# Kernel tuning notes

Hardware: AMD Instinct MI355X
Metric: run time of the kernel (lower is better)

## Reference

```python
import jax, jax.numpy as jnp
import numpy as np

N, IN_F, OUT_F = 2048, 512, 512

def setup_inputs() -> dict:
    key = jax.random.key(0)
    kx, ka, kb = jax.random.split(key, 3)
    x = jax.random.uniform(kx, (N, IN_F), dtype=jnp.float32)          # inputs in [0,1]
    a = jax.random.uniform(ka, (OUT_F, IN_F), dtype=jnp.float32)      # weight in [0,1]
    b = jax.random.uniform(kb, (OUT_F,), dtype=jnp.float32)           # bias in [0,1]
    return {"x": x, "a": a, "b": b}

def reference(x, a, b):
    # Lukasiewicz / max-plus 'matmul':
    # y[n,o] = max(0, max_i(x[n,i] + a[o,i] - 1)), then max with bias b[o].
    inter = x[:, None, :] + a[None, :, :] - 1.0        # [N, out, in]
    y = jnp.maximum(jnp.max(inter, axis=-1), 0.0)      # [N, out]
    y = jnp.maximum(y, b[None, :])
    return y
```

## Files before the change

### kernel.cpp

```cpp
#include <hip/hip_runtime.h>
#include <cstdint>


#define NROW 2048
#define NK   512
#define NCOL 512
#define RPB  8
#define CBL  256
#define KQ   32
typedef float f32x4 __attribute__((ext_vector_type(4)));

__device__ __forceinline__ void async_load16(const float* g, float* l) {
  __builtin_amdgcn_global_load_lds(
      (const __attribute__((address_space(1))) void*)g,
      (__attribute__((address_space(3))) void*)l, 16, 0, 0);
}

__global__ __launch_bounds__(256) void luka_prep(const float* __restrict__ A,
                                                 f32x4* __restrict__ Apc) {
  int idx = blockIdx.x * 256 + threadIdx.x;
  int o  = idx >> 7;
  int k4 = idx & 127;
  int cb = o >> 8, oc = o & 255;
  int c  = oc >> 6, l = oc & 63;
  f32x4 v = *(const f32x4*)(A + o * NK + k4 * 4);
  Apc[((cb * 128 + k4) << 8) + (l << 2) + c] = v;
}

__global__ __launch_bounds__(256) void luka_main(
    const f32x4* __restrict__ Apc, const float* __restrict__ X,
    const float* __restrict__ Bv, float* __restrict__ Y) {
  __shared__ float xsl[RPB * NK];
  __shared__ float red[4 * RPB * CBL];
  const int tid  = threadIdx.x;
  const int lane = tid & 63;
  const int w    = tid >> 6;
  const int colblk  = blockIdx.x;
  const int rowBase = blockIdx.y * RPB;

  {
    const float* Xg = X + (size_t)rowBase * NK;
#pragma unroll
    for (int rnd = 0; rnd < 4; ++rnd) {
      int base = rnd * 256 + w * 64;
      async_load16(Xg + (size_t)(base + lane) * 4, &xsl[base * 4]);
    }
  }

  const f32x4* __restrict__ Aw =
      Apc + (((size_t)(colblk * 128 + w * KQ)) << 8) + (lane << 2);

  float acc[RPB][4];
#pragma unroll
  for (int r = 0; r < RPB; ++r)
#pragma unroll
    for (int c = 0; c < 4; ++c) acc[r][c] = 0.0f;

  f32x4 a0 = __builtin_nontemporal_load(Aw + 0);
  f32x4 a1 = __builtin_nontemporal_load(Aw + 1);
  f32x4 a2 = __builtin_nontemporal_load(Aw + 2);
  f32x4 a3 = __builtin_nontemporal_load(Aw + 3);

  __syncthreads();

#pragma unroll 2
  for (int j = 0; j < KQ; ++j) {
    f32x4 n0, n1, n2, n3;
    if (j + 1 < KQ) {
      const f32x4* p = Aw + ((j + 1) << 8);
      n0 = __builtin_nontemporal_load(p + 0);
      n1 = __builtin_nontemporal_load(p + 1);
      n2 = __builtin_nontemporal_load(p + 2);
      n3 = __builtin_nontemporal_load(p + 3);
    }
    const int kb = (w * KQ + j) * 4;
#pragma unroll
    for (int r = 0; r < RPB; ++r) {
      const f32x4 xv = *(const f32x4*)&xsl[r * NK + kb];
      f32x4 s0 = a0 + xv;
      f32x4 s1 = a1 + xv;
      f32x4 s2 = a2 + xv;
      f32x4 s3 = a3 + xv;
      acc[r][0] = fmaxf(fmaxf(s0.x, s0.y), acc[r][0]);
      acc[r][0] = fmaxf(fmaxf(s0.z, s0.w), acc[r][0]);
      acc[r][1] = fmaxf(fmaxf(s1.x, s1.y), acc[r][1]);
      acc[r][1] = fmaxf(fmaxf(s1.z, s1.w), acc[r][1]);
      acc[r][2] = fmaxf(fmaxf(s2.x, s2.y), acc[r][2]);
      acc[r][2] = fmaxf(fmaxf(s2.z, s2.w), acc[r][2]);
      acc[r][3] = fmaxf(fmaxf(s3.x, s3.y), acc[r][3]);
      acc[r][3] = fmaxf(fmaxf(s3.z, s3.w), acc[r][3]);
    }
    a0 = n0; a1 = n1; a2 = n2; a3 = n3;
  }

#pragma unroll
  for (int r = 0; r < RPB; ++r)
#pragma unroll
    for (int c = 0; c < 4; ++c)
      red[(w * RPB + r) * CBL + c * 64 + lane] = acc[r][c];
  __syncthreads();

  const float bv = Bv[colblk * CBL + tid];
#pragma unroll
  for (int p = 0; p < RPB; ++p) {
    float m = fmaxf(fmaxf(red[(0 * RPB + p) * CBL + tid],
                          red[(1 * RPB + p) * CBL + tid]),
                    fmaxf(red[(2 * RPB + p) * CBL + tid],
                          red[(3 * RPB + p) * CBL + tid]));
    float t = m - 1.0f;
    Y[(size_t)(rowBase + p) * NCOL + colblk * CBL + tid] =
        fmaxf(fmaxf(t, bv), 0.0f);
  }
}

#define TILE 64
#define BK   64
__global__ __launch_bounds__(256) void luka_fb(
    const float* __restrict__ X, const float* __restrict__ A,
    const float* __restrict__ Bv, float* __restrict__ Y) {
  __shared__ float xs[2][TILE * BK];
  __shared__ float as[2][TILE * BK];
  const int tid = threadIdx.x, wave = tid >> 6, tx = tid & 15, ty = tid >> 4;
  const int rowBase = blockIdx.y * TILE, colBase = blockIdx.x * TILE;
  uint32_t xoff[4], aoff[4];
#pragma unroll
  for (int r = 0; r < 4; ++r) {
    int row = ty * 4 + r;
    xoff[r] = (uint32_t)row * 256u + ((uint32_t)((row & 15) ^ (row >> 2)) << 4);
  }
#pragma unroll
  for (int c = 0; c < 4; ++c) {
    int row = tx * 4 + c;
    aoff[c] = (uint32_t)row * 256u + ((uint32_t)((row & 15) ^ (row >> 2)) << 4);
  }
  float acc[4][4];
#pragma unroll
  for (int r = 0; r < 4; ++r)
#pragma unroll
    for (int c = 0; c < 4; ++c) acc[r][c] = 0.0f;
  const int row0 = tid >> 4, sl = tid & 15;
  auto stage = [&](int buf, int kt) {
#pragma unroll
    for (int j = 0; j < 4; ++j) {
      int row = row0 + j * 16;
      int m = (row & 15) ^ (row >> 2);
      int kk = ((sl ^ m) << 2);
      async_load16(X + (size_t)(rowBase + row) * NK + kt * BK + kk,
                   &xs[buf][j * 1024 + wave * 256]);
      async_load16(A + (size_t)(colBase + row) * NK + kt * BK + kk,
                   &as[buf][j * 1024 + wave * 256]);
    }
  };
  stage(0, 0);
  __syncthreads();
  int buf = 0;
#pragma unroll 1
  for (int kt = 0; kt < NK / BK; ++kt) {
    if (kt < NK / BK - 1) stage(buf ^ 1, kt + 1);
    const char* xb = (const char*)&xs[buf][0];
    const char* ab = (const char*)&as[buf][0];
#pragma unroll
    for (int s4 = 0; s4 < BK / 4; ++s4) {
      f32x4 xf[4], af[4];
#pragma unroll
      for (int r = 0; r < 4; ++r)
        xf[r] = *(const f32x4*)(xb + (xoff[r] ^ (uint32_t)(s4 << 4)));
#pragma unroll
      for (int c = 0; c < 4; ++c)
        af[c] = *(const f32x4*)(ab + (aoff[c] ^ (uint32_t)(s4 << 4)));
#pragma unroll
      for (int r = 0; r < 4; ++r)
#pragma unroll
        for (int c = 0; c < 4; ++c) {
          f32x4 s = xf[r] + af[c];
          float t0 = fmaxf(fmaxf(s.x, s.y), acc[r][c]);
          acc[r][c] = fmaxf(fmaxf(s.z, s.w), t0);
        }
    }
    __syncthreads();
    buf ^= 1;
  }
  const f32x4 bv = *(const f32x4*)&Bv[colBase + tx * 4];
  float bvv[4] = {bv.x, bv.y, bv.z, bv.w};
#pragma unroll
  for (int r = 0; r < 4; ++r) {
    f32x4 o;
    o.x = fmaxf(fmaxf(acc[r][0] - 1.0f, bvv[0]), 0.0f);
    o.y = fmaxf(fmaxf(acc[r][1] - 1.0f, bvv[1]), 0.0f);
    o.z = fmaxf(fmaxf(acc[r][2] - 1.0f, bvv[2]), 0.0f);
    o.w = fmaxf(fmaxf(acc[r][3] - 1.0f, bvv[3]), 0.0f);
    *(f32x4*)&Y[(size_t)(rowBase + ty * 4 + r) * NCOL + colBase + tx * 4] = o;
  }
}

extern "C" void kernel_launch(void* const* d_in, const int* in_sizes, int n_in,
                              void* d_out, int out_size, void* d_ws, size_t ws_size,
                              hipStream_t stream) {
  const float* X = (const float*)d_in[0];
  const float* A = (const float*)d_in[1];
  const float* B = (const float*)d_in[2];
  float* Y = (float*)d_out;

  if (ws_size >= (size_t)NCOL * NK * sizeof(float)) {
    f32x4* Apc = (f32x4*)d_ws;
    luka_prep<<<dim3(NCOL * NK / 4 / 256), dim3(256), 0, stream>>>(A, Apc);
    dim3 grid(NCOL / CBL, NROW / RPB);
    luka_main<<<grid, dim3(256), 0, stream>>>(Apc, X, B, Y);
  } else {
    dim3 grid(NCOL / TILE, NROW / TILE);
    luka_fb<<<grid, dim3(256), 0, stream>>>(X, A, B, Y);
  }
}
```

Before: 99.41 us.

## Assign one row per wave over full K, drop LDS cross-wave reduction

Instead of splitting the K dimension across the four waves and reducing their partial maxima through shared memory, each wave now handles one output row over the full K range, with 4 rows per block. This removes the reduction buffer, the second barrier and the strided output pass, and doubles the grid size. In exchange each wave streams the whole A column block with ordinary rather than nontemporal loads, so A traffic per block rises and there is less register-level reuse of each A load across rows.

```diff
diff --git a/kernel.cpp b/kernel.cpp
--- a/kernel.cpp
+++ b/kernel.cpp
@@ -5,9 +5,8 @@
 #define NROW 2048
 #define NK   512
 #define NCOL 512
-#define RPB  8
+#define RPB  4
 #define CBL  256
-#define KQ   32
 typedef float f32x4 __attribute__((ext_vector_type(4)));
 
 __device__ __forceinline__ void async_load16(const float* g, float* l) {
@@ -31,7 +30,6 @@
     const f32x4* __restrict__ Apc, const float* __restrict__ X,
     const float* __restrict__ Bv, float* __restrict__ Y) {
   __shared__ float xsl[RPB * NK];
-  __shared__ float red[4 * RPB * CBL];
   const int tid  = threadIdx.x;
   const int lane = tid & 63;
   const int w    = tid >> 6;
@@ -41,76 +39,54 @@
   {
     const float* Xg = X + (size_t)rowBase * NK;
 #pragma unroll
-    for (int rnd = 0; rnd < 4; ++rnd) {
+    for (int rnd = 0; rnd < 2; ++rnd) {
       int base = rnd * 256 + w * 64;
       async_load16(Xg + (size_t)(base + lane) * 4, &xsl[base * 4]);
     }
   }
 
   const f32x4* __restrict__ Aw =
-      Apc + (((size_t)(colblk * 128 + w * KQ)) << 8) + (lane << 2);
+      Apc + (((size_t)(colblk * 128)) << 8) + (lane << 2);
+  const float* __restrict__ xrow = &xsl[w * NK];
 
-  float acc[RPB][4];
-#pragma unroll
-  for (int r = 0; r < RPB; ++r)
-#pragma unroll
-    for (int c = 0; c < 4; ++c) acc[r][c] = 0.0f;
-
-  f32x4 a0 = __builtin_nontemporal_load(Aw + 0);
-  f32x4 a1 = __builtin_nontemporal_load(Aw + 1);
-  f32x4 a2 = __builtin_nontemporal_load(Aw + 2);
-  f32x4 a3 = __builtin_nontemporal_load(Aw + 3);
+  float acc0 = 0.0f, acc1 = 0.0f, acc2 = 0.0f, acc3 = 0.0f;
 
   __syncthreads();
 
+  f32x4 xv = *(const f32x4*)xrow;
+  f32x4 a0 = Aw[0], a1 = Aw[1], a2 = Aw[2], a3 = Aw[3];
+
 #pragma unroll 2
-  for (int j = 0; j < KQ; ++j) {
-    f32x4 n0, n1, n2, n3;
-    if (j + 1 < KQ) {
+  for (int j = 0; j < NK / 4; ++j) {
+    f32x4 xn, n0, n1, n2, n3;
+    if (j + 1 < NK / 4) {
+      xn = *(const f32x4*)(xrow + (j + 1) * 4);
       const f32x4* p = Aw + ((j + 1) << 8);
-      n0 = __builtin_nontemporal_load(p + 0);
-      n1 = __builtin_nontemporal_load(p + 1);
-      n2 = __builtin_nontemporal_load(p + 2);
-      n3 = __builtin_nontemporal_load(p + 3);
+      n0 = p[0]; n1 = p[1]; n2 = p[2]; n3 = p[3];
     }
-    const int kb = (w * KQ + j) * 4;
-#pragma unroll
-    for (int r = 0; r < RPB; ++r) {
-      const f32x4 xv = *(const f32x4*)&xsl[r * NK + kb];
-      f32x4 s0 = a0 + xv;
-      f32x4 s1 = a1 + xv;
-      f32x4 s2 = a2 + xv;
-      f32x4 s3 = a3 + xv;
-      acc[r][0] = fmaxf(fmaxf(s0.x, s0.y), acc[r][0]);
-      acc[r][0] = fmaxf(fmaxf(s0.z, s0.w), acc[r][0]);
-      acc[r][1] = fmaxf(fmaxf(s1.x, s1.y), acc[r][1]);
-      acc[r][1] = fmaxf(fmaxf(s1.z, s1.w), acc[r][1]);
-      acc[r][2] = fmaxf(fmaxf(s2.x, s2.y), acc[r][2]);
-      acc[r][2] = fmaxf(fmaxf(s2.z, s2.w), acc[r][2]);
-      acc[r][3] = fmaxf(fmaxf(s3.x, s3.y), acc[r][3]);
-      acc[r][3] = fmaxf(fmaxf(s3.z, s3.w), acc[r][3]);
-    }
-    a0 = n0; a1 = n1; a2 = n2; a3 = n3;
+    f32x4 s0 = a0 + xv;
+    f32x4 s1 = a1 + xv;
+    f32x4 s2 = a2 + xv;
+    f32x4 s3 = a3 + xv;
+    acc0 = fmaxf(fmaxf(s0.x, s0.y), acc0);
+    acc0 = fmaxf(fmaxf(s0.z, s0.w), acc0);
+    acc1 = fmaxf(fmaxf(s1.x, s1.y), acc1);
+    acc1 = fmaxf(fmaxf(s1.z, s1.w), acc1);
+    acc2 = fmaxf(fmaxf(s2.x, s2.y), acc2);
+    acc2 = fmaxf(fmaxf(s2.z, s2.w), acc2);
+    acc3 = fmaxf(fmaxf(s3.x, s3.y), acc3);
+    acc3 = fmaxf(fmaxf(s3.z, s3.w), acc3);
+    xv = xn; a0 = n0; a1 = n1; a2 = n2; a3 = n3;
   }
 
-#pragma unroll
-  for (int r = 0; r < RPB; ++r)
-#pragma unroll
-    for (int c = 0; c < 4; ++c)
-      red[(w * RPB + r) * CBL + c * 64 + lane] = acc[r][c];
-  __syncthreads();
-
-  const float bv = Bv[colblk * CBL + tid];
-#pragma unroll
-  for (int p = 0; p < RPB; ++p) {
-    float m = fmaxf(fmaxf(red[(0 * RPB + p) * CBL + tid],
-                          red[(1 * RPB + p) * CBL + tid]),
-                    fmaxf(red[(2 * RPB + p) * CBL + tid],
-                          red[(3 * RPB + p) * CBL + tid]));
-    float t = m - 1.0f;
-    Y[(size_t)(rowBase + p) * NCOL + colblk * CBL + tid] =
-        fmaxf(fmaxf(t, bv), 0.0f);
-  }
+  const int row = rowBase + w;
+  const int cbase = colblk * CBL + lane;
+  float b0 = Bv[cbase], b1 = Bv[cbase + 64], b2 = Bv[cbase + 128],
+        b3 = Bv[cbase + 192];
+  Y[(size_t)row * NCOL + cbase]       = fmaxf(fmaxf(acc0 - 1.0f, b0), 0.0f);
+  Y[(size_t)row * NCOL + cbase + 64]  = fmaxf(fmaxf(acc1 - 1.0f, b1), 0.0f);
+  Y[(size_t)row * NCOL + cbase + 128] = fmaxf(fmaxf(acc2 - 1.0f, b2), 0.0f);
+  Y[(size_t)row * NCOL + cbase + 192] = fmaxf(fmaxf(acc3 - 1.0f, b3), 0.0f);
 }
 
 #define TILE 64
```

New measurement: 173.4 us. 74.4% more time.
